# Optimization experiments

Hardware: AMD Instinct MI355X
Metric: run time of the kernel (lower is better)

Reference implementation:

```python
import jax, jax.numpy as jnp
import numpy as np

N = 32768   # nodes
E = 32768   # edges
ND, ED, GD = 12, 5, 11
H = 64
T = 4
STEPS = 3


def setup_inputs() -> dict:
    key = jax.random.key(0)
    ks = jax.random.split(key, 24)
    s = 0.05
    p = lambda k, sh: (jax.random.normal(k, sh) * s).astype(jnp.float32)
    return dict(
        x=jax.random.normal(ks[0], (N, ND), jnp.float32),
        edge_index=jax.random.randint(ks[1], (2, E), 0, N, jnp.int64),
        edge_attr=jax.random.uniform(ks[2], (E, ED), jnp.float32),
        u=jax.random.normal(ks[3], (1, GD), jnp.float32),
        Wp=p(ks[4], (H, ND + GD)), bp=p(ks[5], (H,)),
        We1=p(ks[6], (H, ED)), be1=p(ks[7], (H,)),
        We2=p(ks[8], (H * H, H)), be2=p(ks[9], (H * H,)),
        root=p(ks[10], (H, H)), conv_b=p(ks[11], (H,)),
        Wih=p(ks[12], (3 * H, H)), bih=p(ks[13], (3 * H,)),
        Whh=p(ks[14], (3 * H, H)), bhh=p(ks[15], (3 * H,)),
        Wd1=p(ks[16], (H, 2 * H + ED)), bd1=p(ks[17], (H,)),
        Wd2=p(ks[18], (H // 2, H)), bd2=p(ks[19], (H // 2,)),
        Wd3=p(ks[20], (T, H // 2)), bd3=p(ks[21], (T,)),
    )


def _forward(x, edge_index, edge_attr, u,
             Wp, bp, We1, be1, We2, be2, root, conv_b,
             Wih, bih, Whh, bhh, Wd1, bd1, Wd2, bd2, Wd3, bd3):
    n = x.shape[0]
    e = edge_attr.shape[0]
    src, dst = edge_index[0], edge_index[1]

    # input projection with broadcast global features (batch=None path)
    u_node = jnp.broadcast_to(u, (n, u.shape[-1]))
    h = jnp.tanh(jnp.concatenate([x, u_node], axis=-1) @ Wp.T + bp)

    # edge MLP -> per-edge (H,H) weight matrices; edge_attr is loop-invariant
    ew = jax.nn.relu(edge_attr @ We1.T + be1) @ We2.T + be2   # (E, H*H)
    ew = ew.reshape(e, H, H)                                   # (E, H, H)

    # mean-aggregation denominators (clamped to 1 like scatter-mean)
    counts = jnp.clip(jax.ops.segment_sum(jnp.ones((e,), h.dtype), dst, num_segments=n), 1.0)

    for _ in range(STEPS):
        # NNConv: gather src features, per-edge matmul, scatter-mean into dst
        msg = jnp.einsum('eh,eho->eo', h[src], ew)             # (E, H)
        agg = jax.ops.segment_sum(msg, dst, num_segments=n) / counts[:, None]
        m = jax.nn.relu(agg + h @ root + conv_b)               # dropout off (eval)
        # GRUCell (torch gate order: r, z, n)
        gi = m @ Wih.T + bih
        gh = h @ Whh.T + bhh
        r = jax.nn.sigmoid(gi[:, :H] + gh[:, :H])
        z = jax.nn.sigmoid(gi[:, H:2 * H] + gh[:, H:2 * H])
        ng = jnp.tanh(gi[:, 2 * H:] + r * gh[:, 2 * H:])
        h = (1.0 - z) * ng + z * h

    # per-edge decoder
    e_in = jnp.concatenate([h[src], h[dst], edge_attr], axis=-1)
    d = jax.nn.relu(e_in @ Wd1.T + bd1)
    d = jax.nn.relu(d @ Wd2.T + bd2)
    return d @ Wd3.T + bd3                                     # (E, T)


def reference(x, edge_index, edge_attr, u,
              Wp, bp, We1, be1, We2, be2, root, conv_b,
              Wih, bih, Whh, bhh, Wd1, bd1, Wd2, bd2, Wd3, bd3):
    return _forward(x, edge_index, edge_attr, u,
                    Wp, bp, We1, be1, We2, be2, root, conv_b,
                    Wih, bih, Whh, bhh, Wd1, bd1, Wd2, bd2, Wd3, bd3)
```

## Files before the change

### kernel.cpp

```cpp
#include <hip/hip_runtime.h>
#include <hip/hip_bf16.h>
#include <stdint.h>


#define N_NODES 32768
#define N_EDGES 32768
#define STEPS 3

typedef __attribute__((ext_vector_type(8))) short short8;
typedef __attribute__((ext_vector_type(4))) float float4v;

__device__ __forceinline__ float bf2f(unsigned short u) {
    union { unsigned int i; float f; } v; v.i = ((unsigned int)u) << 16; return v.f;
}
__device__ __forceinline__ unsigned short f2bf(float f) {
    union { float f; unsigned int i; } v; v.f = f;
    unsigned int x = v.i;
    return (unsigned short)((x + 0x7fffu + ((x >> 16) & 1u)) >> 16);
}

__device__ __forceinline__ void gload_lds16(const void* g, void* l) {
    __builtin_amdgcn_global_load_lds(
        (__attribute__((address_space(1))) void*)g,
        (__attribute__((address_space(3))) void*)l, 16, 0, 0);
}

__global__ __launch_bounds__(256) void k_setup(
    const float* __restrict__ root, const float* __restrict__ Wih,
    const float* __restrict__ Whh,
    const float* __restrict__ We2, const float* __restrict__ be2,
    const float* __restrict__ Wd1, const float* __restrict__ bd1,
    const float* __restrict__ Wd2,
    const float* __restrict__ x, const float* __restrict__ u,
    const float* __restrict__ Wp, const float* __restrict__ bp,
    const float* __restrict__ ea, const float* __restrict__ We1,
    const float* __restrict__ be1,
    unsigned short* __restrict__ rootTf, unsigned short* __restrict__ wcombf,
    unsigned short* __restrict__ w2tf,
    unsigned short* __restrict__ wd1f, unsigned short* __restrict__ wd2f,
    unsigned short* __restrict__ hb,
    unsigned short* __restrict__ hidT, float* __restrict__ cnts)
{
    int b = blockIdx.x, tid = threadIdx.x;
    if (b < 144) {
        int i = b * 256 + tid;
        if (i < 4096) {
            int j = i & 7, lane = (i >> 3) & 63, g = i >> 9;
            int kb = g >> 2, nf = g & 3;
            int o = nf * 16 + (lane & 15);
            int k = kb * 32 + (lane >> 4) * 8 + j;
            rootTf[i] = f2bf(root[k * 64 + o]);
        } else if (i < 4096 + 32768) {
            int t = i - 4096;
            int j = t & 7, lane = (t >> 3) & 63, g = t >> 9;
            int kb = g >> 4, nf = g & 15;
            int cp = nf * 16 + (lane & 15);
            int k = kb * 32 + (lane >> 4) * 8 + j;
            float v;
            if (cp < 128)      v = (k < 64) ? Wih[cp * 64 + k] : Whh[cp * 64 + (k - 64)];
            else if (cp < 192) v = (k < 64) ? Wih[cp * 64 + k] : 0.f;
            else               v = (k < 64) ? 0.f : Whh[(cp - 64) * 64 + (k - 64)];
            wcombf[t] = f2bf(v);
        }
    } else if (b < 1184) {
        int t = (b - 144) * 256 + tid;
        if (t < 65 * 4096) {
            int kk = t >> 12, r = t & 4095;
            int j = r & 7, lane = (r >> 3) & 63, g = r >> 9;
            int half = g >> 2, nf = g & 3;
            int o = nf * 16 + (lane & 15);
            int hh = half * 32 + (lane >> 4) * 8 + j;
            float v = (kk < 64) ? We2[((size_t)(hh * 64 + o)) * 64 + kk]
                                : be2[(size_t)hh * 64 + o];
            w2tf[t] = f2bf(v);
        }
    } else if (b < 1232) {
        int i = (b - 1184) * 256 + tid;
        if (i < 10240) {
            int j = i & 7, lane = (i >> 3) & 63, g = i >> 9;
            int kb = g >> 2, nf = g & 3;
            int o = nf * 16 + (lane & 15);
            int k = kb * 32 + (lane >> 4) * 8 + j;
            float v = (k < 133) ? Wd1[(size_t)o * 133 + k] : (k == 133 ? bd1[o] : 0.f);
            wd1f[i] = f2bf(v);
        } else if (i < 10240 + 2048) {
            int t = i - 10240;
            int j = t & 7, lane = (t >> 3) & 63, g = t >> 9;
            int kb = g >> 1, nf = g & 1;
            int o = nf * 16 + (lane & 15);
            int k = kb * 32 + (lane >> 4) * 8 + j;
            wd2f[t] = f2bf(Wd2[(size_t)o * 64 + k]);
        }
    } else if (b < 9424) {
        int idx = (b - 1232) * 256 + tid;
        int n = idx >> 6, j = idx & 63;
        const float* wr = Wp + j * 23;
        const float* xr = x + (size_t)n * 12;
        float s = bp[j];
#pragma unroll
        for (int i = 0; i < 12; i++) s += xr[i] * wr[i];
#pragma unroll
        for (int i = 0; i < 11; i++) s += u[i] * wr[12 + i];
        hb[idx] = f2bf(tanhf(s));
    } else if (b < 17616) {
        int idx = (b - 9424) * 256 + tid;
        int el = idx & 63, j = (idx >> 6) & 63, eb = idx >> 12;
        int e = eb * 64 + el;
        float s = be1[j];
#pragma unroll
        for (int i = 0; i < 5; i++) s += ea[(size_t)e * 5 + i] * We1[j * 5 + i];
        hidT[(size_t)j * N_EDGES + e] = f2bf(s > 0.f ? s : 0.f);
    } else {
        int idx = (b - 17616) * 1024 + tid * 4;
        if (idx < 32768) {
            float4v z = {0.f, 0.f, 0.f, 0.f};
            *(float4v*)(cnts + idx) = z;
        }
    }
}

__global__ __launch_bounds__(256) void k_counts(
    const int* __restrict__ ei, float* __restrict__ counts)
{
    int i = blockIdx.x * 256 + threadIdx.x;
    if (i < N_EDGES) atomicAdd(&counts[ei[N_EDGES + i]], 1.0f);
}

__global__ __launch_bounds__(1024) void k_scan(
    const float* __restrict__ cnts, int* __restrict__ off, int* __restrict__ woff)
{
    __shared__ int part[1024];
    int t = threadIdx.x;
    int loc[32];
    int s = 0;
#pragma unroll
    for (int i = 0; i < 32; i++) { loc[i] = s; s += (int)cnts[t * 32 + i]; }
    part[t] = s;
    __syncthreads();
    for (int d = 1; d < 1024; d <<= 1) {
        int y = (t >= d) ? part[t - d] : 0;
        __syncthreads();
        part[t] += y;
        __syncthreads();
    }
    int pre = (t == 0) ? 0 : part[t - 1];
#pragma unroll
    for (int i = 0; i < 32; i++) {
        off[t * 32 + i] = pre + loc[i];
        woff[t * 32 + i] = pre + loc[i];
    }
    if (t == 1023) off[32768] = part[1023];
}

__global__ __launch_bounds__(256) void k_scatter(
    const int* __restrict__ ei, int* __restrict__ woff, int* __restrict__ eorder)
{
    int e = blockIdx.x * 256 + threadIdx.x;
    if (e < N_EDGES) {
        int d = ei[N_EDGES + e];
        int slot = atomicAdd(&woff[d], 1);
        eorder[slot] = e;
    }
}

__global__ __launch_bounds__(256, 2) void k_msg_fused(
    const unsigned short* __restrict__ hidT,
    const unsigned short* __restrict__ hb,
    const unsigned short* __restrict__ w2tf,
    const int* __restrict__ ei,
    float* __restrict__ msgbuf)
{
    __shared__ __attribute__((aligned(16))) unsigned char smem[73728];
    unsigned short* stg = (unsigned short*)smem;
    unsigned short* hvl = (unsigned short*)(smem + 65536);
    float* red = (float*)smem;

    int tid = threadIdx.x, w = tid >> 6, lane = tid & 63;
    int l15 = lane & 15, quad = lane >> 4;
    int ebase = blockIdx.x * 64;
    int n = 16 + (w == 3 ? 1 : 0);

    {
        const unsigned short* hp = hidT + (size_t)(w * 16) * N_EDGES + ebase + lane;
        unsigned short* dp = hvl + (w * 16) * 64 + lane;
#pragma unroll
        for (int r = 0; r < 16; r++)
            dp[r * 64] = hp[(size_t)r * N_EDGES];
    }
    short8 afr[4][2];
#pragma unroll
    for (int t = 0; t < 4; t++) {
        int src = ei[ebase + t * 16 + l15];
#pragma unroll
        for (int hh = 0; hh < 2; hh++)
            afr[t][hh] = *(const short8*)(hb + (size_t)src * 64 + hh * 32 + quad * 8);
    }

    unsigned short* wbuf = stg + w * (2 * 4096);
    auto stage = [&](int r, int db) {
        const unsigned short* g = w2tf + (size_t)(w * 16 + r) * 4096;
        unsigned short* d = wbuf + db * 4096;
#pragma unroll
        for (int c = 0; c < 8; c++)
            gload_lds16(g + (size_t)c * 512 + lane * 8, d + c * 512);
    };

    stage(0, 0);
    stage(1, 1);

    float4v acc[4][4] = {};
    for (int r = 0; r < n; r++) {
        int db = r & 1;
        if (r < n - 1) { asm volatile("s_waitcnt vmcnt(8)" ::: "memory"); }
        else           { asm volatile("s_waitcnt vmcnt(0)" ::: "memory"); }

        short8 bfr[2][4];
        const unsigned short* bb = wbuf + db * 4096;
#pragma unroll
        for (int hh = 0; hh < 2; hh++)
#pragma unroll
            for (int nf = 0; nf < 4; nf++)
                bfr[hh][nf] = *(const short8*)(bb + (hh * 4 + nf) * 512 + lane * 8);

        bool bias = (r == 16);
        unsigned long long hu[4] = {0ull, 0ull, 0ull, 0ull};
        if (!bias) {
#pragma unroll
            for (int t = 0; t < 4; t++)
                hu[t] = *(const unsigned long long*)(hvl + (w * 16 + r) * 64 + t * 16 + quad * 4);
        }

        asm volatile("s_waitcnt lgkmcnt(0)" ::: "memory");
        if (r + 2 < n) stage(r + 2, db);

#pragma unroll
        for (int t = 0; t < 4; t++) {
            float4v T[4];
#pragma unroll
            for (int nf = 0; nf < 4; nf++) {
                float4v z = {0.f, 0.f, 0.f, 0.f};
                T[nf] = __builtin_amdgcn_mfma_f32_16x16x32_bf16(afr[t][0], bfr[0][nf], z, 0, 0, 0);
            }
#pragma unroll
            for (int nf = 0; nf < 4; nf++)
                T[nf] = __builtin_amdgcn_mfma_f32_16x16x32_bf16(afr[t][1], bfr[1][nf], T[nf], 0, 0, 0);
#pragma unroll
            for (int rr = 0; rr < 4; rr++) {
                float hvv = bias ? 1.0f : bf2f((unsigned short)(hu[t] >> (16 * rr)));
#pragma unroll
                for (int nf = 0; nf < 4; nf++)
                    acc[t][nf][rr] += hvv * T[nf][rr];
            }
        }
    }

    __syncthreads();
    float* rp = red + w * 4224;
#pragma unroll
    for (int t = 0; t < 4; t++)
#pragma unroll
        for (int nf = 0; nf < 4; nf++)
#pragma unroll
            for (int rr = 0; rr < 4; rr++)
                rp[(t * 16 + quad * 4 + rr) * 66 + nf * 16 + l15] = acc[t][nf][rr];
    __syncthreads();
    {
        int row = tid >> 2, cg = tid & 3;
        float s[16];
#pragma unroll
        for (int k = 0; k < 16; k++) {
            float v = 0.f;
#pragma unroll
            for (int ww = 0; ww < 4; ww++)
                v += red[ww * 4224 + row * 66 + cg * 16 + k];
            s[k] = v;
        }
        float* op = msgbuf + (size_t)(ebase + row) * 64 + cg * 16;
#pragma unroll
        for (int q = 0; q < 4; q++) {
            float4v v4 = { s[4 * q], s[4 * q + 1], s[4 * q + 2], s[4 * q + 3] };
            *(float4v*)(op + 4 * q) = v4;
        }
    }
}

__global__ __launch_bounds__(256) void k_node(
    const unsigned short* __restrict__ hb_in,
    const unsigned short* __restrict__ rootTf,
    const unsigned short* __restrict__ wcombf,
    const float* __restrict__ msgbuf, const int* __restrict__ off,
    const int* __restrict__ eorder,
    const float* __restrict__ counts,
    const float* __restrict__ conv_b,
    const float* __restrict__ bih, const float* __restrict__ bhh,
    unsigned short* __restrict__ hb_out)
{
    __shared__ unsigned short m_lds[64 * 72];
    __shared__ float aggl[64 * 68];
    int tid = threadIdx.x, w = tid >> 6, lane = tid & 63;
    int l15 = lane & 15, quad = lane >> 4;
    int node0 = blockIdx.x * 64;
    int row0 = w * 16;

    {
        int nl = tid >> 2, cg = tid & 3;
        int nn = node0 + nl;
        int s0 = off[nn], s1 = off[nn + 1];
        float acc[16] = {};
        for (int sl = s0; sl < s1; sl++) {
            int e = eorder[sl];
            const float* mr = msgbuf + (size_t)e * 64 + cg * 16;
#pragma unroll
            for (int q = 0; q < 4; q++) {
                float4v v = *(const float4v*)(mr + 4 * q);
#pragma unroll
                for (int j = 0; j < 4; j++) acc[4 * q + j] += v[j];
            }
        }
#pragma unroll
        for (int k = 0; k < 16; k++) aggl[nl * 68 + cg * 16 + k] = acc[k];
    }
    __syncthreads();

    float4v acc1[4] = {};
    {
        short8 a1[2];
#pragma unroll
        for (int kb = 0; kb < 2; kb++)
            a1[kb] = *(const short8*)(hb_in + (size_t)(node0 + row0 + l15) * 64 + kb * 32 + quad * 8);
#pragma unroll
        for (int kb = 0; kb < 2; kb++)
#pragma unroll
            for (int nf = 0; nf < 4; nf++) {
                short8 b = *(const short8*)(rootTf + (size_t)((kb * 4 + nf) * 64 + lane) * 8);
                acc1[nf] = __builtin_amdgcn_mfma_f32_16x16x32_bf16(a1[kb], b, acc1[nf], 0, 0, 0);
            }
    }
#pragma unroll
    for (int rr = 0; rr < 4; rr++) {
        int nl = row0 + quad * 4 + rr;
        float cnt = counts[node0 + nl]; if (cnt < 1.f) cnt = 1.f;
        float rcp = 1.f / cnt;
#pragma unroll
        for (int nf = 0; nf < 4; nf++) {
            int c = nf * 16 + l15;
            float av = aggl[nl * 68 + c];
            float mv = av * rcp + acc1[nf][rr] + conv_b[c];
            m_lds[nl * 72 + c] = f2bf(mv > 0.f ? mv : 0.f);
        }
    }
    __syncthreads();

    float4v acc2[16] = {};
#pragma unroll
    for (int kb = 0; kb < 4; kb++) {
        short8 a2;
        if (kb < 2)
            a2 = *(const short8*)(m_lds + (row0 + l15) * 72 + kb * 32 + quad * 8);
        else
            a2 = *(const short8*)(hb_in + (size_t)(node0 + row0 + l15) * 64 + (kb - 2) * 32 + quad * 8);
#pragma unroll
        for (int nf = 0; nf < 16; nf++) {
            short8 b = *(const short8*)(wcombf + (size_t)((kb * 16 + nf) * 64 + lane) * 8);
            acc2[nf] = __builtin_amdgcn_mfma_f32_16x16x32_bf16(a2, b, acc2[nf], 0, 0, 0);
        }
    }

#pragma unroll
    for (int nf0 = 0; nf0 < 4; nf0++) {
        int c = nf0 * 16 + l15;
        float br = bih[c] + bhh[c];
        float bz = bih[64 + c] + bhh[64 + c];
        float bni = bih[128 + c], bnh = bhh[128 + c];
#pragma unroll
        for (int rr = 0; rr < 4; rr++) {
            int node = node0 + row0 + quad * 4 + rr;
            float gr = 1.f / (1.f + __expf(-(acc2[nf0][rr] + br)));
            float gz = 1.f / (1.f + __expf(-(acc2[nf0 + 4][rr] + bz)));
            float ng = tanhf(acc2[nf0 + 8][rr] + bni + gr * (acc2[nf0 + 12][rr] + bnh));
            float ho = bf2f(hb_in[(size_t)node * 64 + c]);
            float hn = (1.f - gz) * ng + gz * ho;
            hb_out[(size_t)node * 64 + c] = f2bf(hn);
        }
    }
}

__global__ __launch_bounds__(256) void k_decoder(
    const unsigned short* __restrict__ hb, const int* __restrict__ ei,
    const float* __restrict__ ea,
    const unsigned short* __restrict__ wd1f, const unsigned short* __restrict__ wd2f,
    const float* __restrict__ bd2,
    const float* __restrict__ Wd3, const float* __restrict__ bd3,
    float* __restrict__ out)
{
    __shared__ unsigned short d1f[4][1024];
    __shared__ float d2s[4][16 * 33];
    int tid = threadIdx.x, w = tid >> 6, lane = tid & 63;
    int l15 = lane & 15, quad = lane >> 4;
    int ebase = blockIdx.x * 64 + w * 16;
    int e = ebase + l15;
    int src = ei[e], dst = ei[N_EDGES + e];

    short8 a[5];
#pragma unroll
    for (int kb = 0; kb < 2; kb++) {
        a[kb]     = *(const short8*)(hb + (size_t)src * 64 + kb * 32 + quad * 8);
        a[2 + kb] = *(const short8*)(hb + (size_t)dst * 64 + kb * 32 + quad * 8);
    }
    {
        union { short8 v; unsigned short u[8]; } tea;
#pragma unroll
        for (int j = 0; j < 8; j++) {
            float vv = 0.f;
            if (quad == 0) vv = (j < 5) ? ea[(size_t)e * 5 + j] : (j == 5 ? 1.f : 0.f);
            tea.u[j] = f2bf(vv);
        }
        a[4] = tea.v;
    }

    float4v acc1[4] = {};
#pragma unroll
    for (int kb = 0; kb < 5; kb++)
#pragma unroll
        for (int nf = 0; nf < 4; nf++) {
            short8 b = *(const short8*)(wd1f + (size_t)((kb * 4 + nf) * 64 + lane) * 8);
            acc1[nf] = __builtin_amdgcn_mfma_f32_16x16x32_bf16(a[kb], b, acc1[nf], 0, 0, 0);
        }
#pragma unroll
    for (int nf = 0; nf < 4; nf++) {
        int kbp = nf >> 1;
        int lanep_hi = ((nf & 1) * 2 + (l15 >> 3)) * 16;
        int jp = l15 & 7;
#pragma unroll
        for (int r = 0; r < 4; r++) {
            float v = acc1[nf][r];
            d1f[w][kbp * 512 + (lanep_hi + quad * 4 + r) * 8 + jp] = f2bf(v > 0.f ? v : 0.f);
        }
    }
    float4v acc2[2] = {};
#pragma unroll
    for (int kb = 0; kb < 2; kb++) {
        short8 a2 = *(const short8*)(&d1f[w][kb * 512 + lane * 8]);
#pragma unroll
        for (int nf = 0; nf < 2; nf++) {
            short8 b = *(const short8*)(wd2f + (size_t)((kb * 2 + nf) * 64 + lane) * 8);
            acc2[nf] = __builtin_amdgcn_mfma_f32_16x16x32_bf16(a2, b, acc2[nf], 0, 0, 0);
        }
    }
#pragma unroll
    for (int nf = 0; nf < 2; nf++) {
        int c = nf * 16 + l15;
        float bias = bd2[c];
#pragma unroll
        for (int r = 0; r < 4; r++) {
            float v = acc2[nf][r] + bias;
            d2s[w][(quad * 4 + r) * 33 + c] = v > 0.f ? v : 0.f;
        }
    }
    {
        int e_l = lane >> 2, t = lane & 3;
        float s = bd3[t];
        const float* w3 = Wd3 + t * 32;
        const float* dr = &d2s[w][e_l * 33];
#pragma unroll
        for (int k = 0; k < 32; k++) s += w3[k] * dr[k];
        out[(size_t)(ebase + e_l) * 4 + t] = s;
    }
}

extern "C" void kernel_launch(void* const* d_in, const int* in_sizes, int n_in,
                              void* d_out, int out_size, void* d_ws, size_t ws_size,
                              hipStream_t stream)
{
    const float* x      = (const float*)d_in[0];
    const int*   ei     = (const int*)d_in[1];
    const float* ea     = (const float*)d_in[2];
    const float* u      = (const float*)d_in[3];
    const float* Wp     = (const float*)d_in[4];
    const float* bp     = (const float*)d_in[5];
    const float* We1    = (const float*)d_in[6];
    const float* be1    = (const float*)d_in[7];
    const float* We2    = (const float*)d_in[8];
    const float* be2    = (const float*)d_in[9];
    const float* root   = (const float*)d_in[10];
    const float* conv_b = (const float*)d_in[11];
    const float* Wih    = (const float*)d_in[12];
    const float* bih    = (const float*)d_in[13];
    const float* Whh    = (const float*)d_in[14];
    const float* bhh    = (const float*)d_in[15];
    const float* Wd1    = (const float*)d_in[16];
    const float* bd1    = (const float*)d_in[17];
    const float* Wd2    = (const float*)d_in[18];
    const float* bd2    = (const float*)d_in[19];
    const float* Wd3    = (const float*)d_in[20];
    const float* bd3    = (const float*)d_in[21];
    float* out = (float*)d_out;

    char* ws = (char*)d_ws;
    size_t off_b = 0;
    auto take = [&](size_t bytes) -> char* {
        char* p = ws + off_b; off_b = (off_b + bytes + 255) & ~(size_t)255; return p;
    };
    unsigned short* hb     = (unsigned short*)take((size_t)N_NODES * 64 * 2);
    unsigned short* hidT   = (unsigned short*)take((size_t)N_EDGES * 64 * 2);
    float*          msgbuf = (float*)take((size_t)N_EDGES * 64 * 4);
    float*          cnts   = (float*)take((size_t)N_NODES * 4);
    int*            off    = (int*)take((size_t)(N_NODES + 1) * 4);
    int*            woff   = (int*)take((size_t)N_NODES * 4);
    int*            eorder = (int*)take((size_t)N_EDGES * 4);
    unsigned short* w2tf   = (unsigned short*)take((size_t)66 * 4096 * 2);
    unsigned short* rootTf = (unsigned short*)take((size_t)4096 * 2);
    unsigned short* wcombf = (unsigned short*)take((size_t)32768 * 2);
    unsigned short* wd1f   = (unsigned short*)take((size_t)10240 * 2);
    unsigned short* wd2f   = (unsigned short*)take((size_t)2048 * 2);
    (void)ws_size;

    k_setup<<<17648, 256, 0, stream>>>(root, Wih, Whh, We2, be2, Wd1, bd1, Wd2,
                                       x, u, Wp, bp, ea, We1, be1,
                                       rootTf, wcombf, w2tf, wd1f, wd2f,
                                       hb, hidT, cnts);
    k_counts<<<128, 256, 0, stream>>>(ei, cnts);
    k_scan<<<1, 1024, 0, stream>>>(cnts, off, woff);
    k_scatter<<<128, 256, 0, stream>>>(ei, woff, eorder);

    for (int s = 0; s < STEPS; s++) {
        k_msg_fused<<<N_EDGES / 64, 256, 0, stream>>>(hidT, hb, w2tf, ei, msgbuf);
        k_node<<<N_NODES / 64, 256, 0, stream>>>(hb, rootTf, wcombf, msgbuf, off,
                                                 eorder, cnts, conv_b, bih, bhh, hb);
    }
    k_decoder<<<N_EDGES / 64, 256, 0, stream>>>(hb, ei, ea, wd1f, wd2f, bd2,
                                                Wd3, bd3, out);
}
```

Before: 262.2 us.

## Share staged edge-weight tiles across two edge groups in 512-thread message blocks

Measured after the change: 271.8 us. 3.7% more time.

```diff
diff --git a/kernel.cpp b/kernel.cpp
--- a/kernel.cpp
+++ b/kernel.cpp
@@ -163,124 +163,123 @@
     }
 }
 
-__global__ __launch_bounds__(256, 2) void k_msg_fused(
+__global__ __launch_bounds__(512, 2) void k_msg_fused(
     const unsigned short* __restrict__ hidT,
     const unsigned short* __restrict__ hb,
     const unsigned short* __restrict__ w2tf,
     const int* __restrict__ ei,
     float* __restrict__ msgbuf)
 {
-    __shared__ __attribute__((aligned(16))) unsigned char smem[73728];
+    __shared__ __attribute__((aligned(16))) unsigned char smem[81920];
     unsigned short* stg = (unsigned short*)smem;
     unsigned short* hvl = (unsigned short*)(smem + 65536);
     float* red = (float*)smem;
 
     int tid = threadIdx.x, w = tid >> 6, lane = tid & 63;
     int l15 = lane & 15, quad = lane >> 4;
-    int ebase = blockIdx.x * 64;
-    int n = 16 + (w == 3 ? 1 : 0);
-
-    {
-        const unsigned short* hp = hidT + (size_t)(w * 16) * N_EDGES + ebase + lane;
-        unsigned short* dp = hvl + (w * 16) * 64 + lane;
-#pragma unroll
-        for (int r = 0; r < 16; r++)
-            dp[r * 64] = hp[(size_t)r * N_EDGES];
+    int kg = w & 3, eg = w >> 2;
+    int ebase = blockIdx.x * 128;
+    int n_w = 16 + (kg == 3 ? 1 : 0);
+
+#pragma unroll
+    for (int i = 0; i < 8; i++) {
+        int row = w * 8 + i;
+        unsigned int v = *((const unsigned int*)(hidT + (size_t)row * N_EDGES + ebase) + lane);
+        *((unsigned int*)hvl + row * 64 + lane) = v;
     }
     short8 afr[4][2];
 #pragma unroll
     for (int t = 0; t < 4; t++) {
-        int src = ei[ebase + t * 16 + l15];
+        int src = ei[ebase + eg * 64 + t * 16 + l15];
 #pragma unroll
         for (int hh = 0; hh < 2; hh++)
             afr[t][hh] = *(const short8*)(hb + (size_t)src * 64 + hh * 32 + quad * 8);
     }
 
-    unsigned short* wbuf = stg + w * (2 * 4096);
     auto stage = [&](int r, int db) {
-        const unsigned short* g = w2tf + (size_t)(w * 16 + r) * 4096;
-        unsigned short* d = wbuf + db * 4096;
-#pragma unroll
-        for (int c = 0; c < 8; c++)
-            gload_lds16(g + (size_t)c * 512 + lane * 8, d + c * 512);
+        const unsigned short* g = w2tf + (size_t)(kg * 16 + r) * 4096;
+        unsigned short* d = stg + (kg * 2 + db) * 4096;
+#pragma unroll
+        for (int c = 0; c < 4; c++) {
+            int ch = eg * 4 + c;
+            gload_lds16(g + ch * 512 + lane * 8, d + ch * 512);
+        }
     };
 
     stage(0, 0);
     stage(1, 1);
+    asm volatile("s_waitcnt lgkmcnt(0)" ::: "memory");
+    __builtin_amdgcn_s_barrier();
 
     float4v acc[4][4] = {};
-    for (int r = 0; r < n; r++) {
+    for (int r = 0; r <= 16; r++) {
         int db = r & 1;
-        if (r < n - 1) { asm volatile("s_waitcnt vmcnt(8)" ::: "memory"); }
-        else           { asm volatile("s_waitcnt vmcnt(0)" ::: "memory"); }
-
+        if (r >= n_w - 1) { asm volatile("s_waitcnt vmcnt(0)" ::: "memory"); }
+        else              { asm volatile("s_waitcnt vmcnt(4)" ::: "memory"); }
+        __builtin_amdgcn_s_barrier();
+
+        bool act = (r < n_w);
         short8 bfr[2][4];
-        const unsigned short* bb = wbuf + db * 4096;
-#pragma unroll
-        for (int hh = 0; hh < 2; hh++)
-#pragma unroll
-            for (int nf = 0; nf < 4; nf++)
-                bfr[hh][nf] = *(const short8*)(bb + (hh * 4 + nf) * 512 + lane * 8);
-
+        unsigned long long hu[4] = {0ull, 0ull, 0ull, 0ull};
         bool bias = (r == 16);
-        unsigned long long hu[4] = {0ull, 0ull, 0ull, 0ull};
-        if (!bias) {
-#pragma unroll
-            for (int t = 0; t < 4; t++)
-                hu[t] = *(const unsigned long long*)(hvl + (w * 16 + r) * 64 + t * 16 + quad * 4);
-        }
-
+        if (act) {
+            const unsigned short* bb = stg + (kg * 2 + db) * 4096;
+#pragma unroll
+            for (int hh = 0; hh < 2; hh++)
+#pragma unroll
+                for (int nf = 0; nf < 4; nf++)
+                    bfr[hh][nf] = *(const short8*)(bb + (hh * 4 + nf) * 512 + lane * 8);
+            if (!bias) {
+#pragma unroll
+                for (int t = 0; t < 4; t++)
+                    hu[t] = *(const unsigned long long*)(hvl + (kg * 16 + r) * 128 + eg * 64 + t * 16 + quad * 4);
+            }
+        }
         asm volatile("s_waitcnt lgkmcnt(0)" ::: "memory");
-        if (r + 2 < n) stage(r + 2, db);
-
-#pragma unroll
-        for (int t = 0; t < 4; t++) {
-            float4v T[4];
-#pragma unroll
-            for (int nf = 0; nf < 4; nf++) {
-                float4v z = {0.f, 0.f, 0.f, 0.f};
-                T[nf] = __builtin_amdgcn_mfma_f32_16x16x32_bf16(afr[t][0], bfr[0][nf], z, 0, 0, 0);
+        __builtin_amdgcn_s_barrier();
+        if (r + 2 < n_w) stage(r + 2, db);
+
+        if (act) {
+#pragma unroll
+            for (int t = 0; t < 4; t++) {
+                float4v T[4];
+#pragma unroll
+                for (int nf = 0; nf < 4; nf++) {
+                    float4v z = {0.f, 0.f, 0.f, 0.f};
+                    T[nf] = __builtin_amdgcn_mfma_f32_16x16x32_bf16(afr[t][0], bfr[0][nf], z, 0, 0, 0);
+                }
+#pragma unroll
+                for (int nf = 0; nf < 4; nf++)
+                    T[nf] = __builtin_amdgcn_mfma_f32_16x16x32_bf16(afr[t][1], bfr[1][nf], T[nf], 0, 0, 0);
+#pragma unroll
+                for (int rr = 0; rr < 4; rr++) {
+                    float hvv = bias ? 1.0f : bf2f((unsigned short)(hu[t] >> (16 * rr)));
+#pragma unroll
+                    for (int nf = 0; nf < 4; nf++)
+                        acc[t][nf][rr] += hvv * T[nf][rr];
+                }
             }
-#pragma unroll
-            for (int nf = 0; nf < 4; nf++)
-                T[nf] = __builtin_amdgcn_mfma_f32_16x16x32_bf16(afr[t][1], bfr[1][nf], T[nf], 0, 0, 0);
-#pragma unroll
-            for (int rr = 0; rr < 4; rr++) {
-                float hvv = bias ? 1.0f : bf2f((unsigned short)(hu[t] >> (16 * rr)));
-#pragma unroll
-                for (int nf = 0; nf < 4; nf++)
-                    acc[t][nf][rr] += hvv * T[nf][rr];
-            }
-        }
-    }
-
-    __syncthreads();
-    float* rp = red + w * 4224;
-#pragma unroll
-    for (int t = 0; t < 4; t++)
-#pragma unroll
-        for (int nf = 0; nf < 4; nf++)
+        }
+    }
+
+    int row_w = tid >> 2, kq = tid & 3;
+#pragma unroll
+    for (int nf = 0; nf < 4; nf++) {
+        __syncthreads();
+#pragma unroll
+        for (int t = 0; t < 4; t++)
 #pragma unroll
             for (int rr = 0; rr < 4; rr++)
-                rp[(t * 16 + quad * 4 + rr) * 66 + nf * 16 + l15] = acc[t][nf][rr];
-    __syncthreads();
-    {
-        int row = tid >> 2, cg = tid & 3;
-        float s[16];
-#pragma unroll
-        for (int k = 0; k < 16; k++) {
-            float v = 0.f;
-#pragma unroll
-            for (int ww = 0; ww < 4; ww++)
-                v += red[ww * 4224 + row * 66 + cg * 16 + k];
-            s[k] = v;
-        }
-        float* op = msgbuf + (size_t)(ebase + row) * 64 + cg * 16;
-#pragma unroll
-        for (int q = 0; q < 4; q++) {
-            float4v v4 = { s[4 * q], s[4 * q + 1], s[4 * q + 2], s[4 * q + 3] };
-            *(float4v*)(op + 4 * q) = v4;
-        }
+                red[kg * 2304 + (eg * 64 + t * 16 + quad * 4 + rr) * 18 + l15] = acc[t][nf][rr];
+        __syncthreads();
+        float4v s = {0.f, 0.f, 0.f, 0.f};
+#pragma unroll
+        for (int g2 = 0; g2 < 4; g2++) {
+            const float* rp = red + g2 * 2304 + row_w * 18 + kq * 4;
+#pragma unroll
+            for (int j = 0; j < 4; j++) s[j] += rp[j];
+        }
+        *(float4v*)(msgbuf + (size_t)(ebase + row_w) * 64 + nf * 16 + kq * 4) = s;
     }
 }
 
@@ -524,7 +523,7 @@
     k_scatter<<<128, 256, 0, stream>>>(ei, woff, eorder);
 
     for (int s = 0; s < STEPS; s++) {
-        k_msg_fused<<<N_EDGES / 64, 256, 0, stream>>>(hidT, hb, w2tf, ei, msgbuf);
+        k_msg_fused<<<N_EDGES / 128, 512, 0, stream>>>(hidT, hb, w2tf, ei, msgbuf);
         k_node<<<N_NODES / 64, 256, 0, stream>>>(hb, rootTf, wcombf, msgbuf, off,
                                                  eorder, cnts, conv_b, bih, bhh, hb);
     }
```
